# Kernel optimization log

Measured on AMD Instinct MI355X. Metric: run time of the kernel, lower is better.

Reference implementation:

```python
import jax, jax.numpy as jnp
import numpy as np

B, W, F_IN = 128, 128, 64   # batch, window_size, num_features
N = 64                      # nodes per graph == num_features == tcn_out_channels
E = 4096                    # edges per graph
ED = 16                     # edge_feature_dim
H, C = 4, 32                # heads, gat_out_dim
FLAT = N * H * C            # 8192
HID = FLAT // 4             # 2048
LRELU_SLOPE = 0.01          # F.leaky_relu default
BN_EPS = 1e-5


def setup_inputs() -> dict:
    key = jax.random.key(0)
    ks = jax.random.split(key, 16)
    x = jax.random.normal(ks[0], (B, W, F_IN), jnp.float32)
    edge_index = jax.random.randint(ks[1], (2, E), 0, N)
    edge_attr = jax.random.normal(ks[2], (B, E, ED), jnp.float32)
    s = lambda k, shape, fan: jax.random.normal(k, shape, jnp.float32) / np.sqrt(fan)
    tcn_w = s(ks[3], (N, F_IN, 3), F_IN * 3)
    tcn_b = jnp.zeros((N,), jnp.float32)
    lin_l_w = s(ks[4], (H * C, W), W)
    lin_l_b = jnp.zeros((H * C,), jnp.float32)
    lin_e_w = s(ks[5], (H * C, ED), ED)
    lin_e_b = jnp.zeros((H * C,), jnp.float32)
    att = s(ks[6], (1, H, C), C)
    fc1_w = s(ks[7], (HID, FLAT), FLAT)
    fc1_b = jnp.zeros((HID,), jnp.float32)
    bn_g = jnp.ones((HID,), jnp.float32)
    bn_b = jnp.zeros((HID,), jnp.float32)
    fc2_w = s(ks[8], (2, HID), HID)
    fc2_b = jnp.zeros((2,), jnp.float32)
    return dict(x=x, edge_index=edge_index, edge_attr=edge_attr,
                tcn_w=tcn_w, tcn_b=tcn_b,
                lin_l_w=lin_l_w, lin_l_b=lin_l_b,
                lin_e_w=lin_e_w, lin_e_b=lin_e_b, att=att,
                fc1_w=fc1_w, fc1_b=fc1_b, bn_g=bn_g, bn_b=bn_b,
                fc2_w=fc2_w, fc2_b=fc2_b)


def reference(x, edge_index, edge_attr, tcn_w, tcn_b,
              lin_l_w, lin_l_b, lin_e_w, lin_e_b, att,
              fc1_w, fc1_b, bn_g, bn_b, fc2_w, fc2_b):
    # TCN: Conv1d(k=3, pad=1) over the window dim
    xt = jnp.transpose(x, (0, 2, 1))  # [B, F_IN, W]
    x_g = jax.lax.conv_general_dilated(
        xt, tcn_w, window_strides=(1,), padding=((1, 1),),
        dimension_numbers=('NCH', 'OIH', 'NCH')) + tcn_b[None, :, None]
    # x_g: [B, N, W] -> per-sample graph with N nodes, W-dim node features

    src, dst = edge_index[0], edge_index[1]

    def gat_one(xn, ea):
        # xn: [N, W], ea: [E, ED]
        h = (xn @ lin_l_w.T + lin_l_b).reshape(N, H, C)
        e = (ea @ lin_e_w.T + lin_e_b).reshape(E, H, C)
        xi = h[dst]               # [E, H, C] target node feats
        xj = h[src]               # [E, H, C] source node feats
        a = jax.nn.leaky_relu(xi + xj + e, LRELU_SLOPE)
        score = jnp.einsum('ehc,ohc->eh', a, att)  # [E, H]
        # segment softmax over edges grouped by destination node
        m = jax.ops.segment_max(score, dst, num_segments=N)
        m = jnp.where(jnp.isfinite(m), m, 0.0)
        ex = jnp.exp(score - m[dst])
        den = jax.ops.segment_sum(ex, dst, num_segments=N)
        alpha = ex / (den[dst] + 1e-16)            # [E, H]
        msg = xj * alpha[:, :, None]               # [E, H, C]
        out = jax.ops.segment_sum(msg, dst, num_segments=N)  # [N, H, C]
        return out.reshape(N, H * C)

    x_gat = jax.vmap(gat_one)(x_g, edge_attr)      # [B, N, H*C]
    x_gat = jax.nn.elu(x_gat)
    x_flat = x_gat.reshape(B, FLAT)

    h1 = x_flat @ fc1_w.T + fc1_b
    # BatchNorm1d in eval mode with fresh running stats (mean=0, var=1)
    h1 = h1 * (bn_g / jnp.sqrt(1.0 + BN_EPS)) + bn_b
    h1 = jax.nn.relu(h1)  # dropout is identity in eval
    logits = h1 @ fc2_w.T + fc2_b
    return logits
```

## Files before the change

### kernel.cpp

```cpp
#include <hip/hip_runtime.h>
#include <math.h>

#define BB   128
#define WW   128
#define FIN  64
#define NNODE 64
#define NE   4096
#define EDIM 16
#define NH   4
#define CDIM 32
#define HC   128
#define FLATD 8192
#define HIDD 2048

#define OFF_H    0u
#define OFF_P    1048576u
#define OFF_XGB  3211264u
#define OFF_BK   4259840u

typedef unsigned short u16;
typedef u16    u16x8  __attribute__((ext_vector_type(8)));
typedef u16    u16x4  __attribute__((ext_vector_type(4)));
typedef __bf16 bf16x8 __attribute__((ext_vector_type(8)));
typedef float  f32x4  __attribute__((ext_vector_type(4)));
typedef float  f32x16 __attribute__((ext_vector_type(16)));

__device__ __forceinline__ u16 f2bf(float f) {
    unsigned u = __float_as_uint(f);
    u += 0x7fffu + ((u >> 16) & 1u);
    return (u16)(u >> 16);
}
__device__ __forceinline__ void hilo(float v, u16* h, u16* l) {
    u16 hh = f2bf(v);
    float hf = __uint_as_float(((unsigned)hh) << 16);
    *h = hh;
    *l = f2bf(v - hf);
}

__global__ __launch_bounds__(256) void k01(
        const float* __restrict__ x, const float* __restrict__ tcn_w,
        const float* __restrict__ tcn_b, const float* __restrict__ lin_l_w,
        const float* __restrict__ lin_l_b, float* __restrict__ h,
        const int* __restrict__ ei, int* __restrict__ bstart,
        int* __restrict__ blist)
{
    __shared__ float xs[130*65];
    __shared__ float xg[32*132];
    __shared__ float tw[32*192];
    __shared__ int cnt[64];
    __shared__ int cur[65];
    const int bid = blockIdx.x, t = threadIdx.x;

    if (bid == 256) {
        if (t < 64) cnt[t] = 0;
        __syncthreads();
        for (int e = t; e < NE; e += 256) atomicAdd(&cnt[ei[NE + e]], 1);
        __syncthreads();
        if (t == 0) {
            int run = 0;
            for (int n = 0; n < 64; ++n) { cur[n] = run; run += cnt[n]; }
            cur[64] = run;
        }
        __syncthreads();
        if (t < 65) bstart[t] = cur[t];
        __syncthreads();
        for (int e = t; e < NE; e += 256) {
            int d = ei[NE + e], s = ei[e];
            int p = atomicAdd(&cur[d], 1);
            blist[p] = (e << 12) | (d << 6) | s;
        }
        return;
    }

    const int b = bid >> 1, half = bid & 1;
    const int n0 = half * 32;

    for (int idx = t; idx < 8192; idx += 256) {
        int w = idx >> 6, i = idx & 63;
        xs[(w+1)*65 + i] = x[b*8192 + idx];
    }
    {
        const float4* src = (const float4*)(tcn_w + n0*192);
        for (int idx = t; idx < 1536; idx += 256)
            ((float4*)tw)[idx] = src[idx];
    }
    if (t < 65) { xs[t] = 0.f; xs[129*65 + t] = 0.f; }
    __syncthreads();

    {
        const int nl = t >> 3;
        const int n  = n0 + nl;
        const int w0 = (t & 7) * 16;
        float acc[16];
        const float tb = tcn_b[n];
#pragma unroll
        for (int j = 0; j < 16; ++j) acc[j] = tb;
        for (int i = 0; i < 64; ++i) {
            const float t0 = tw[nl*192 + 3*i + 0];
            const float t1 = tw[nl*192 + 3*i + 1];
            const float t2 = tw[nl*192 + 3*i + 2];
            float a = xs[(w0+0)*65 + i];
            float c0 = xs[(w0+1)*65 + i];
#pragma unroll
            for (int dw = 0; dw < 16; ++dw) {
                float c = xs[(w0+dw+2)*65 + i];
                acc[dw] += a*t0 + c0*t1 + c*t2;
                a = c0; c0 = c;
            }
        }
#pragma unroll
        for (int dw = 0; dw < 16; ++dw) xg[nl*132 + w0 + dw] = acc[dw];
    }
    __syncthreads();

    {
        const int o2 = t & 63, ng = t >> 6;
        const int oA = o2, oB = o2 + 64;
        float accA[8], accB[8];
        const float lbA = lin_l_b[oA], lbB = lin_l_b[oB];
#pragma unroll
        for (int j = 0; j < 8; ++j) { accA[j] = lbA; accB[j] = lbB; }
        for (int c = 0; c < 32; ++c) {
            const float4 lwA = *(const float4*)&lin_l_w[oA*128 + c*4];
            const float4 lwB = *(const float4*)&lin_l_w[oB*128 + c*4];
#pragma unroll
            for (int nn = 0; nn < 8; ++nn) {
                const float4 xv = *(const float4*)&xg[(ng*8+nn)*132 + c*4];
                accA[nn] += xv.x*lwA.x + xv.y*lwA.y + xv.z*lwA.z + xv.w*lwA.w;
                accB[nn] += xv.x*lwB.x + xv.y*lwB.y + xv.z*lwB.z + xv.w*lwB.w;
            }
        }
#pragma unroll
        for (int nn = 0; nn < 8; ++nn) {
            const int n = n0 + ng*8 + nn;
            h[(b*64 + n)*128 + oA] = accA[nn];
            h[(b*64 + n)*128 + oB] = accB[nn];
        }
    }
}

#define CAPF 2560
__global__ __launch_bounds__(512, 1) void k2_fused(
        const float* __restrict__ hbase, const float* __restrict__ ea,
        const float* __restrict__ lin_e_w, const float* __restrict__ lin_e_b,
        const float* __restrict__ att, const int* __restrict__ bstart,
        const int* __restrict__ blist, u16* __restrict__ xgb)
{
    __shared__ float hbuf[64*132];
    __shared__ float scl[CAPF*4];
    __shared__ float Pm[4][32][68];
    __shared__ int   bst[33];
    const int b = blockIdx.x, half = blockIdx.y, t = threadIdx.x;
    const int lane = t & 63, wv = t >> 6, l32 = lane & 31, h5 = lane >> 5;

    const int lo  = bstart[half*32];
    const int cnt = min(bstart[half*32 + 32] - lo, CAPF);
    const int gcnt = (cnt + 31) >> 5;

    int g = wv;
    int pkc = 0; bool validc = false;
    float4 v0c = {0.f,0.f,0.f,0.f}, v1c = {0.f,0.f,0.f,0.f};
    if (g < gcnt) {
        const int idx0 = g*32 + l32;
        validc = idx0 < cnt;
        pkc = validc ? blist[lo + idx0] : 0;
        const float* eap = ea + ((size_t)b*NE + (size_t)(pkc >> 12))*16 + h5*8;
        v0c = *(const float4*)eap;
        v1c = *(const float4*)(eap + 4);
    }

    for (int idx = t; idx < 2048; idx += 512) {
        const int row = idx >> 5, c4 = (idx & 31) * 4;
        float4 hv = *(const float4*)&hbase[(size_t)b*8192 + row*128 + c4];
        const float4 eb = *(const float4*)&lin_e_b[c4];
        hv.x += 0.5f*eb.x; hv.y += 0.5f*eb.y;
        hv.z += 0.5f*eb.z; hv.w += 0.5f*eb.w;
        *(float4*)&hbuf[row*132 + c4] = hv;
    }
    {
        const f32x4 z4 = {0.f, 0.f, 0.f, 0.f};
        for (int idx = t; idx < 4*32*68/4; idx += 512) ((f32x4*)Pm)[idx] = z4;
    }
    if (t < 33) bst[t] = bstart[half*32 + t];
    bf16x8 Ah[4], Al[4];
#pragma unroll
    for (int mt = 0; mt < 4; ++mt) {
        const float* wp = &lin_e_w[(mt*32 + l32)*16 + h5*8];
        const float4 w0 = *(const float4*)wp;
        const float4 w1 = *(const float4*)(wp + 4);
        u16 th[8], tl[8];
        hilo(w0.x,&th[0],&tl[0]); hilo(w0.y,&th[1],&tl[1]);
        hilo(w0.z,&th[2],&tl[2]); hilo(w0.w,&th[3],&tl[3]);
        hilo(w1.x,&th[4],&tl[4]); hilo(w1.y,&th[5],&tl[5]);
        hilo(w1.z,&th[6],&tl[6]); hilo(w1.w,&th[7],&tl[7]);
        u16x8 vh = { th[0],th[1],th[2],th[3],th[4],th[5],th[6],th[7] };
        u16x8 vl = { tl[0],tl[1],tl[2],tl[3],tl[4],tl[5],tl[6],tl[7] };
        Ah[mt] = *(bf16x8*)&vh;
        Al[mt] = *(bf16x8*)&vl;
    }
    float4 attv[4][4];
#pragma unroll
    for (int mt = 0; mt < 4; ++mt)
#pragma unroll
        for (int gq = 0; gq < 4; ++gq)
            attv[mt][gq] = *(const float4*)&att[mt*32 + gq*8 + h5*4];
    __syncthreads();

    while (g < gcnt) {
        const int gn = g + 8;
        const int pk = pkc; const bool valid = validc;
        const float4 v0 = v0c, v1 = v1c;
        const int idx = g*32 + l32;
        if (gn < gcnt) {
            const int idxn = gn*32 + l32;
            validc = idxn < cnt;
            pkc = validc ? blist[lo + idxn] : 0;
            const float* eap = ea + ((size_t)b*NE + (size_t)(pkc >> 12))*16 + h5*8;
            v0c = *(const float4*)eap;
            v1c = *(const float4*)(eap + 4);
        } else {
            validc = false;
        }
        const int sn = pk & 63, dd = (pk >> 6) & 63;
        u16 bh[8], bl[8];
        hilo(v0.x,&bh[0],&bl[0]); hilo(v0.y,&bh[1],&bl[1]);
        hilo(v0.z,&bh[2],&bl[2]); hilo(v0.w,&bh[3],&bl[3]);
        hilo(v1.x,&bh[4],&bl[4]); hilo(v1.y,&bh[5],&bl[5]);
        hilo(v1.z,&bh[6],&bl[6]); hilo(v1.w,&bh[7],&bl[7]);
        u16x8 vbh = { bh[0],bh[1],bh[2],bh[3],bh[4],bh[5],bh[6],bh[7] };
        u16x8 vbl = { bl[0],bl[1],bl[2],bl[3],bl[4],bl[5],bl[6],bl[7] };
        const bf16x8 Bh = *(bf16x8*)&vbh;
        const bf16x8 Bl = *(bf16x8*)&vbl;
        float hacc[4];
#pragma unroll
        for (int mt = 0; mt < 4; ++mt) {
            f32x16 D = {0.f,0.f,0.f,0.f,0.f,0.f,0.f,0.f,
                        0.f,0.f,0.f,0.f,0.f,0.f,0.f,0.f};
            D = __builtin_amdgcn_mfma_f32_32x32x16_bf16(Al[mt], Bh, D, 0, 0, 0);
            D = __builtin_amdgcn_mfma_f32_32x32x16_bf16(Ah[mt], Bl, D, 0, 0, 0);
            D = __builtin_amdgcn_mfma_f32_32x32x16_bf16(Ah[mt], Bh, D, 0, 0, 0);
            float s = 0.f;
#pragma unroll
            for (int g4 = 0; g4 < 4; ++g4) {
                const int ob = mt*32 + g4*8 + h5*4;
                const float4 hd = *(const float4*)&hbuf[dd*132 + ob];
                const float4 hs = *(const float4*)&hbuf[sn*132 + ob];
                float x0 = hd.x + hs.x + D[g4*4+0];
                float x1 = hd.y + hs.y + D[g4*4+1];
                float x2 = hd.z + hs.z + D[g4*4+2];
                float x3 = hd.w + hs.w + D[g4*4+3];
                x0 = fmaxf(x0, 0.01f*x0); x1 = fmaxf(x1, 0.01f*x1);
                x2 = fmaxf(x2, 0.01f*x2); x3 = fmaxf(x3, 0.01f*x3);
                const float4 a4 = attv[mt][g4];
                s += a4.x*x0 + a4.y*x1 + a4.z*x2 + a4.w*x3;
            }
            hacc[mt] = s;
        }
#pragma unroll
        for (int hh = 0; hh < 4; ++hh)
            hacc[hh] += __shfl_xor(hacc[hh], 32);
        if (h5 == 0 && valid)
            *(float4*)&scl[idx*4] = make_float4(hacc[0], hacc[1], hacc[2], hacc[3]);
        g = gn;
    }
    __syncthreads();

    {
        const int pair = t >> 2, sub = t & 3;
        const int nl = pair >> 2, hh = pair & 3;
        const int s0 = bst[nl] - lo, s1 = bst[nl+1] - lo;
        float mx = -3.4e38f;
        for (int i = s0 + sub; i < s1; i += 4) mx = fmaxf(mx, scl[i*4 + hh]);
        mx = fmaxf(mx, __shfl_xor(mx, 1));
        mx = fmaxf(mx, __shfl_xor(mx, 2));
        float den = 0.f;
        for (int i = s0 + sub; i < s1; i += 4) {
            const float ex = __expf(scl[i*4 + hh] - mx);
            scl[i*4 + hh] = ex;
            den += ex;
        }
        den += __shfl_xor(den, 1);
        den += __shfl_xor(den, 2);
        const float rd = 1.0f / (den + 1e-16f);
        for (int i = s0 + sub; i < s1; i += 4) {
            const int src = blist[lo + i] & 63;
            atomicAdd(&Pm[hh][nl][src], scl[i*4 + hh] * rd);
        }
    }
    __syncthreads();

    {
        const int hh = wv >> 1, ct = wv & 1;
        const int l16 = lane & 15, q = lane >> 4;
        const int cb = hh*32 + ct*16 + l16;
        const float lb2 = 0.5f * lin_e_b[cb];
        bf16x8 Hh2[2], Hl2[2];
#pragma unroll
        for (int kk = 0; kk < 2; ++kk) {
            u16 hhv[8], hlv[8];
#pragma unroll
            for (int i = 0; i < 8; ++i) {
                const float v = hbuf[(kk*32 + q*8 + i)*132 + cb];
                hilo(v, &hhv[i], &hlv[i]);
            }
            u16x8 vhh = { hhv[0],hhv[1],hhv[2],hhv[3],hhv[4],hhv[5],hhv[6],hhv[7] };
            u16x8 vhl = { hlv[0],hlv[1],hlv[2],hlv[3],hlv[4],hlv[5],hlv[6],hlv[7] };
            Hh2[kk] = *(bf16x8*)&vhh;
            Hl2[kk] = *(bf16x8*)&vhl;
        }
#pragma unroll
        for (int mrow = 0; mrow < 32; mrow += 16) {
            f32x4 D = {0.f, 0.f, 0.f, 0.f};
#pragma unroll
            for (int kk = 0; kk < 2; ++kk) {
                const float* pp = &Pm[hh][mrow + l16][kk*32 + q*8];
                const float4 a0 = *(const float4*)pp;
                const float4 a1 = *(const float4*)(pp + 4);
                u16 ph[8], pl[8];
                hilo(a0.x,&ph[0],&pl[0]); hilo(a0.y,&ph[1],&pl[1]);
                hilo(a0.z,&ph[2],&pl[2]); hilo(a0.w,&ph[3],&pl[3]);
                hilo(a1.x,&ph[4],&pl[4]); hilo(a1.y,&ph[5],&pl[5]);
                hilo(a1.z,&ph[6],&pl[6]); hilo(a1.w,&ph[7],&pl[7]);
                u16x8 vph = { ph[0],ph[1],ph[2],ph[3],ph[4],ph[5],ph[6],ph[7] };
                u16x8 vpl = { pl[0],pl[1],pl[2],pl[3],pl[4],pl[5],pl[6],pl[7] };
                const bf16x8 Ph = *(bf16x8*)&vph, Pl = *(bf16x8*)&vpl;
                D = __builtin_amdgcn_mfma_f32_16x16x32_bf16(Pl, Hh2[kk], D, 0, 0, 0);
                D = __builtin_amdgcn_mfma_f32_16x16x32_bf16(Ph, Hl2[kk], D, 0, 0, 0);
                D = __builtin_amdgcn_mfma_f32_16x16x32_bf16(Ph, Hh2[kk], D, 0, 0, 0);
            }
#pragma unroll
            for (int r = 0; r < 4; ++r) {
                const int m = mrow + q*4 + r;
                const float corr = (bst[m+1] > bst[m]) ? lb2 : 0.f;
                float v = D[r] - corr;
                v = v > 0.f ? v : expm1f(v);
                xgb[(size_t)b*8192 + (half*32 + m)*128 + cb] = f2bf(v);
            }
        }
    }
}

__global__ __launch_bounds__(256) void k3_fc1(
        const u16* __restrict__ xgb, const float* __restrict__ fc1_w,
        float* __restrict__ part)
{
    __shared__ u16 Ash[128*72];
    __shared__ u16 Bsh[32*72];
    const int jb = blockIdx.x, ks = blockIdx.y, t = threadIdx.x;
    const int j0 = jb*32, k0 = ks*1024;
    const int wave = t >> 6, lane = t & 63;
    const int quad = lane >> 4, l16 = lane & 15;
    const int wm = (wave & 1) * 64, wn = (wave >> 1) * 16;

    f32x4 acc[4];
#pragma unroll
    for (int i = 0; i < 4; ++i) acc[i] = (f32x4){0.f, 0.f, 0.f, 0.f};

    const int arow = t >> 1, acol = (t & 1) * 32;
    const int brow = t >> 3, bcol = (t & 7) * 8;

    u16x8 Ar[4]; float4 Br0, Br1;
    {
        const u16* ap = xgb + (size_t)arow*FLATD + k0 + acol;
#pragma unroll
        for (int qq = 0; qq < 4; ++qq) Ar[qq] = *(const u16x8*)(ap + qq*8);
        const float* bp = fc1_w + (size_t)(j0 + brow)*FLATD + k0 + bcol;
        Br0 = *(const float4*)bp; Br1 = *(const float4*)(bp + 4);
    }

    for (int kc = 0; kc < 1024; kc += 64) {
#pragma unroll
        for (int qq = 0; qq < 4; ++qq)
            *(u16x8*)&Ash[arow*72 + acol + qq*8] = Ar[qq];
        {
            u16x8 u = { f2bf(Br0.x), f2bf(Br0.y), f2bf(Br0.z), f2bf(Br0.w),
                        f2bf(Br1.x), f2bf(Br1.y), f2bf(Br1.z), f2bf(Br1.w) };
            *(u16x8*)&Bsh[brow*72 + bcol] = u;
        }
        __syncthreads();
        if (kc + 64 < 1024) {
            const u16* ap = xgb + (size_t)arow*FLATD + k0 + kc + 64 + acol;
#pragma unroll
            for (int qq = 0; qq < 4; ++qq) Ar[qq] = *(const u16x8*)(ap + qq*8);
            const float* bp = fc1_w + (size_t)(j0 + brow)*FLATD + k0 + kc + 64 + bcol;
            Br0 = *(const float4*)bp; Br1 = *(const float4*)(bp + 4);
        }
#pragma unroll
        for (int kk = 0; kk < 64; kk += 32) {
            bf16x8 af[4], bfr;
#pragma unroll
            for (int i = 0; i < 4; ++i)
                af[i] = *(const bf16x8*)&Ash[(wm + i*16 + l16)*72 + kk + quad*8];
            bfr = *(const bf16x8*)&Bsh[(wn + l16)*72 + kk + quad*8];
#pragma unroll
            for (int i = 0; i < 4; ++i)
                acc[i] = __builtin_amdgcn_mfma_f32_16x16x32_bf16(af[i], bfr, acc[i], 0, 0, 0);
        }
        __syncthreads();
    }
#pragma unroll
    for (int i = 0; i < 4; ++i) {
        const int n = j0 + wn + l16;
#pragma unroll
        for (int r = 0; r < 4; ++r) {
            const int m = wm + i*16 + quad*4 + r;
            part[(size_t)ks*262144 + (size_t)m*HIDD + n] = acc[i][r];
        }
    }
}

__global__ __launch_bounds__(256) void k4_fc2(
        const float* __restrict__ part, const float* __restrict__ fc1_b,
        const float* __restrict__ bn_g, const float* __restrict__ bn_b,
        const float* __restrict__ fc2_w, const float* __restrict__ fc2_b,
        float* __restrict__ out)
{
    __shared__ float r0[256], r1[256];
    const int b = blockIdx.x, t = threadIdx.x;
    const float inv = 1.0f / sqrtf(1.0f + 1e-5f);
    float p0 = 0.f, p1 = 0.f;
    for (int j = t; j < 2048; j += 256) {
        float hv = 0.f;
#pragma unroll
        for (int s = 0; s < 8; ++s) hv += part[(size_t)s*262144 + (size_t)b*2048 + j];
        float v = (hv + fc1_b[j]) * (bn_g[j] * inv) + bn_b[j];
        v = fmaxf(v, 0.f);
        p0 += v * fc2_w[j];
        p1 += v * fc2_w[2048 + j];
    }
    r0[t] = p0; r1[t] = p1;
    __syncthreads();
    for (int s = 128; s > 0; s >>= 1) {
        if (t < s) { r0[t] += r0[t+s]; r1[t] += r1[t+s]; }
        __syncthreads();
    }
    if (t == 0) {
        out[b*2 + 0] = r0[0] + fc2_b[0];
        out[b*2 + 1] = r1[0] + fc2_b[1];
    }
}

extern "C" void kernel_launch(void* const* d_in, const int* in_sizes, int n_in,
                              void* d_out, int out_size, void* d_ws, size_t ws_size,
                              hipStream_t stream)
{
    const float* x       = (const float*)d_in[0];
    const int*   ei      = (const int*)  d_in[1];
    const float* ea      = (const float*)d_in[2];
    const float* tcn_w   = (const float*)d_in[3];
    const float* tcn_b   = (const float*)d_in[4];
    const float* lin_l_w = (const float*)d_in[5];
    const float* lin_l_b = (const float*)d_in[6];
    const float* lin_e_w = (const float*)d_in[7];
    const float* lin_e_b = (const float*)d_in[8];
    const float* att     = (const float*)d_in[9];
    const float* fc1_w   = (const float*)d_in[10];
    const float* fc1_b   = (const float*)d_in[11];
    const float* bn_g    = (const float*)d_in[12];
    const float* bn_b    = (const float*)d_in[13];
    const float* fc2_w   = (const float*)d_in[14];
    const float* fc2_b   = (const float*)d_in[15];

    float* ws     = (float*)d_ws;
    float* hbuf   = ws + OFF_H;
    float* part   = ws + OFF_P;
    u16*   xgb    = (u16*)(ws + OFF_XGB);
    int*   bstart = (int*)(ws + OFF_BK);
    int*   blist  = bstart + 80;
    float* out    = (float*)d_out;

    k01    <<<257, 256, 0, stream>>>(x, tcn_w, tcn_b, lin_l_w, lin_l_b, hbuf,
                                     ei, bstart, blist);
    k2_fused<<<dim3(BB, 2), 512, 0, stream>>>(hbuf, ea, lin_e_w, lin_e_b, att,
                                              bstart, blist, xgb);
    k3_fc1 <<<dim3(64, 8), 256, 0, stream>>>(xgb, fc1_w, part);
    k4_fc2 <<<BB, 256, 0, stream>>>(part, fc1_b, bn_g, bn_b, fc2_w, fc2_b, out);
}
```

Baseline: 233.4 us.

## Gather node features via one-hot MFMA and split heads across wave groups

Replaces the per-edge LDS gathers of destination and source node features with MFMA products between split-bf16 node-feature fragments held in registers and a one-hot selector built from the dst/src indices. Self-loops get a weight of two. The 8 waves are regrouped into two groups of four, each handling two of the four heads for the same edge groups. This halves per-wave weight registers but makes each edge group's hilo conversion and index loads happen twice. The aim is to remove scattered LDS reads on the edge-score path, at the cost of 8 extra MFMAs per head and extra register pressure from the preloaded fragments.

```diff
diff --git a/kernel.cpp b/kernel.cpp
--- a/kernel.cpp
+++ b/kernel.cpp
@@ -19,11 +19,11 @@
 #define OFF_BK   4259840u
 
 typedef unsigned short u16;
-typedef u16    u16x8  __attribute__((ext_vector_type(8)));
-typedef u16    u16x4  __attribute__((ext_vector_type(4)));
-typedef __bf16 bf16x8 __attribute__((ext_vector_type(8)));
-typedef float  f32x4  __attribute__((ext_vector_type(4)));
-typedef float  f32x16 __attribute__((ext_vector_type(16)));
+typedef u16      u16x8 __attribute__((ext_vector_type(8)));
+typedef unsigned u32x4 __attribute__((ext_vector_type(4)));
+typedef __bf16   bf16x8 __attribute__((ext_vector_type(8)));
+typedef float    f32x4  __attribute__((ext_vector_type(4)));
+typedef float    f32x16 __attribute__((ext_vector_type(16)));
 
 __device__ __forceinline__ u16 f2bf(float f) {
     unsigned u = __float_as_uint(f);
@@ -152,12 +152,13 @@
     __shared__ int   bst[33];
     const int b = blockIdx.x, half = blockIdx.y, t = threadIdx.x;
     const int lane = t & 63, wv = t >> 6, l32 = lane & 31, h5 = lane >> 5;
+    const int pg = wv >> 2, wsub = wv & 3;
 
     const int lo  = bstart[half*32];
     const int cnt = min(bstart[half*32 + 32] - lo, CAPF);
     const int gcnt = (cnt + 31) >> 5;
 
-    int g = wv;
+    int g = wsub;
     int pkc = 0; bool validc = false;
     float4 v0c = {0.f,0.f,0.f,0.f}, v1c = {0.f,0.f,0.f,0.f};
     if (g < gcnt) {
@@ -182,9 +183,10 @@
         for (int idx = t; idx < 4*32*68/4; idx += 512) ((f32x4*)Pm)[idx] = z4;
     }
     if (t < 33) bst[t] = bstart[half*32 + t];
-    bf16x8 Ah[4], Al[4];
-#pragma unroll
-    for (int mt = 0; mt < 4; ++mt) {
+    bf16x8 Ah[2], Al[2];
+#pragma unroll
+    for (int m2 = 0; m2 < 2; ++m2) {
+        const int mt = 2*pg + m2;
         const float* wp = &lin_e_w[(mt*32 + l32)*16 + h5*8];
         const float4 w0 = *(const float4*)wp;
         const float4 w1 = *(const float4*)(wp + 4);
@@ -195,19 +197,36 @@
         hilo(w1.z,&th[6],&tl[6]); hilo(w1.w,&th[7],&tl[7]);
         u16x8 vh = { th[0],th[1],th[2],th[3],th[4],th[5],th[6],th[7] };
         u16x8 vl = { tl[0],tl[1],tl[2],tl[3],tl[4],tl[5],tl[6],tl[7] };
-        Ah[mt] = *(bf16x8*)&vh;
-        Al[mt] = *(bf16x8*)&vl;
-    }
-    float4 attv[4][4];
-#pragma unroll
-    for (int mt = 0; mt < 4; ++mt)
+        Ah[m2] = *(bf16x8*)&vh;
+        Al[m2] = *(bf16x8*)&vl;
+    }
+    float4 attv[2][4];
+#pragma unroll
+    for (int m2 = 0; m2 < 2; ++m2)
 #pragma unroll
         for (int gq = 0; gq < 4; ++gq)
-            attv[mt][gq] = *(const float4*)&att[mt*32 + gq*8 + h5*4];
+            attv[m2][gq] = *(const float4*)&att[(2*pg + m2)*32 + gq*8 + h5*4];
     __syncthreads();
 
+    bf16x8 HA[2][4], LA[2][4];
+#pragma unroll
+    for (int m2 = 0; m2 < 2; ++m2) {
+        const int o = (2*pg + m2)*32 + l32;
+#pragma unroll
+        for (int c = 0; c < 4; ++c) {
+            u16 th[8], tl[8];
+#pragma unroll
+            for (int j = 0; j < 8; ++j)
+                hilo(hbuf[(c*16 + h5*8 + j)*132 + o], &th[j], &tl[j]);
+            u16x8 vh = { th[0],th[1],th[2],th[3],th[4],th[5],th[6],th[7] };
+            u16x8 vl = { tl[0],tl[1],tl[2],tl[3],tl[4],tl[5],tl[6],tl[7] };
+            HA[m2][c] = *(bf16x8*)&vh;
+            LA[m2][c] = *(bf16x8*)&vl;
+        }
+    }
+
     while (g < gcnt) {
-        const int gn = g + 8;
+        const int gn = g + 4;
         const int pk = pkc; const bool valid = validc;
         const float4 v0 = v0c, v1 = v1c;
         const int idx = g*32 + l32;
@@ -221,7 +240,7 @@
         } else {
             validc = false;
         }
-        const int sn = pk & 63, dd = (pk >> 6) & 63;
+        const int sn0 = pk & 63, dd = (pk >> 6) & 63;
         u16 bh[8], bl[8];
         hilo(v0.x,&bh[0],&bl[0]); hilo(v0.y,&bh[1],&bl[1]);
         hilo(v0.z,&bh[2],&bl[2]); hilo(v0.w,&bh[3],&bl[3]);
@@ -231,36 +250,52 @@
         u16x8 vbl = { bl[0],bl[1],bl[2],bl[3],bl[4],bl[5],bl[6],bl[7] };
         const bf16x8 Bh = *(bf16x8*)&vbh;
         const bf16x8 Bl = *(bf16x8*)&vbl;
-        float hacc[4];
-#pragma unroll
-        for (int mt = 0; mt < 4; ++mt) {
+        const unsigned ddp = (dd == sn0) ? 0x4000u : 0x3F80u;
+        const int      sne = (dd == sn0) ? 0x7FFFFFF0 : sn0;
+        bf16x8 zf[4];
+#pragma unroll
+        for (int c = 0; c < 4; ++c) {
+            const int base = c*16 + h5*8;
+            const unsigned ud = (unsigned)(dd - base);
+            const unsigned us = (unsigned)(sne - base);
+            const unsigned wd = ddp << ((ud & 1) << 4);
+            const unsigned wsv = 0x3F80u << ((us & 1) << 4);
+            u32x4 zz;
+#pragma unroll
+            for (int i = 0; i < 4; ++i)
+                zz[i] = (((ud >> 1) == (unsigned)i) ? wd : 0u)
+                      | (((us >> 1) == (unsigned)i) ? wsv : 0u);
+            zf[c] = *(bf16x8*)&zz;
+        }
+        float hacc[2];
+#pragma unroll
+        for (int m2 = 0; m2 < 2; ++m2) {
             f32x16 D = {0.f,0.f,0.f,0.f,0.f,0.f,0.f,0.f,
                         0.f,0.f,0.f,0.f,0.f,0.f,0.f,0.f};
-            D = __builtin_amdgcn_mfma_f32_32x32x16_bf16(Al[mt], Bh, D, 0, 0, 0);
-            D = __builtin_amdgcn_mfma_f32_32x32x16_bf16(Ah[mt], Bl, D, 0, 0, 0);
-            D = __builtin_amdgcn_mfma_f32_32x32x16_bf16(Ah[mt], Bh, D, 0, 0, 0);
+            D = __builtin_amdgcn_mfma_f32_32x32x16_bf16(Al[m2], Bh, D, 0, 0, 0);
+            D = __builtin_amdgcn_mfma_f32_32x32x16_bf16(Ah[m2], Bl, D, 0, 0, 0);
+            D = __builtin_amdgcn_mfma_f32_32x32x16_bf16(Ah[m2], Bh, D, 0, 0, 0);
+#pragma unroll
+            for (int c = 0; c < 4; ++c) {
+                D = __builtin_amdgcn_mfma_f32_32x32x16_bf16(LA[m2][c], zf[c], D, 0, 0, 0);
+                D = __builtin_amdgcn_mfma_f32_32x32x16_bf16(HA[m2][c], zf[c], D, 0, 0, 0);
+            }
             float s = 0.f;
 #pragma unroll
             for (int g4 = 0; g4 < 4; ++g4) {
-                const int ob = mt*32 + g4*8 + h5*4;
-                const float4 hd = *(const float4*)&hbuf[dd*132 + ob];
-                const float4 hs = *(const float4*)&hbuf[sn*132 + ob];
-                float x0 = hd.x + hs.x + D[g4*4+0];
-                float x1 = hd.y + hs.y + D[g4*4+1];
-                float x2 = hd.z + hs.z + D[g4*4+2];
-                float x3 = hd.w + hs.w + D[g4*4+3];
+                float x0 = D[g4*4+0], x1 = D[g4*4+1];
+                float x2 = D[g4*4+2], x3 = D[g4*4+3];
                 x0 = fmaxf(x0, 0.01f*x0); x1 = fmaxf(x1, 0.01f*x1);
                 x2 = fmaxf(x2, 0.01f*x2); x3 = fmaxf(x3, 0.01f*x3);
-                const float4 a4 = attv[mt][g4];
+                const float4 a4 = attv[m2][g4];
                 s += a4.x*x0 + a4.y*x1 + a4.z*x2 + a4.w*x3;
             }
-            hacc[mt] = s;
-        }
-#pragma unroll
-        for (int hh = 0; hh < 4; ++hh)
-            hacc[hh] += __shfl_xor(hacc[hh], 32);
+            hacc[m2] = s;
+        }
+        hacc[0] += __shfl_xor(hacc[0], 32);
+        hacc[1] += __shfl_xor(hacc[1], 32);
         if (h5 == 0 && valid)
-            *(float4*)&scl[idx*4] = make_float4(hacc[0], hacc[1], hacc[2], hacc[3]);
+            *(float2*)&scl[idx*4 + pg*2] = make_float2(hacc[0], hacc[1]);
         g = gn;
     }
     __syncthreads();
```

After: 249.2 us. 6.8% more time.
